# Optimization experiments

Measured on AMD Instinct MI355X. Metric: run time of the kernel, lower is better.

## Reference

```python
import jax, jax.numpy as jnp
import numpy as np

FREQUENCY_COUNT = 16

def setup_inputs() -> dict:
    key = jax.random.key(0)
    k1, k2 = jax.random.split(key)
    x = jax.random.normal(k1, (4096, 1024), dtype=jnp.float32)
    coef = jax.random.normal(k2, (1024, 1024, 2 * FREQUENCY_COUNT + 1), dtype=jnp.float32) * 0.1
    return {"x": x, "coef": coef}

def _fourier_features(x, K):
    ks = jnp.arange(1, K + 1, dtype=x.dtype)            # [K]
    ang = x[:, :, None] * ks[None, None, :]             # [B, I, K]
    ones = jnp.ones(x.shape + (1,), dtype=x.dtype)      # [B, I, 1]
    return jnp.concatenate([jnp.sin(ang), jnp.cos(ang), ones], axis=2)

def reference(x, coef):
    K = (coef.shape[-1] - 1) // 2
    values = _fourier_features(x, K)                     # [B, I, 2K+1]
    # sum over input dim i and frequency dim k, weighted per output j
    return jnp.einsum("oik,bik->bo", coef, values)      # [B, O]
```

## Files before the change

### kernel.cpp

```cpp
#include <hip/hip_runtime.h>


#define O_COLS 1024
#define I_DIM  1024
#define NFW    32
#define NF33   33
#define NIB    16
#define KPW    (NIB * NFW * 64)
#define CW_BYTES ((size_t)O_COLS * KPW * 2)

typedef _Float16 half8 __attribute__((ext_vector_type(8)));
typedef float float4v __attribute__((ext_vector_type(4)));
union H8 { half8 v; _Float16 h[8]; };

__device__ __forceinline__ void gload16(const void* g, void* l) {
  typedef const __attribute__((address_space(1))) unsigned int GU;
  typedef __attribute__((address_space(3))) unsigned int LU;
  __builtin_amdgcn_global_load_lds((GU*)g, (LU*)l, 16, 0, 0);
}

__device__ __forceinline__ int ksrc_of(int f) {
  return (f >= 32) ? 32 : ((f >> 1) + ((f & 1) ? 16 : 0));
}

__global__ __launch_bounds__(64)
void convert_coef(const float* __restrict__ coef, _Float16* __restrict__ Cw,
                  float* __restrict__ bias) {
  const int bid = blockIdx.x;
  const int o = bid >> 4;
  const int ib = bid & 15;
  const int j = threadIdx.x;
  const int i = ib * 64 + j;

  const float* src = coef + (size_t)o * (I_DIM * NF33) + (size_t)i * NF33;
  float r[NF33];
#pragma unroll
  for (int kk = 0; kk < NF33; ++kk) r[kk] = src[kk];

  const int c = j >> 3, e = j & 7;
  const int jswz = ((c ^ (o & 7)) << 3) + e;
  _Float16* dst = Cw + (size_t)o * KPW + (size_t)ib * (NFW * 64) + jswz;
#pragma unroll
  for (int f = 0; f < NFW; ++f) {
    dst[f * 64] = (_Float16)r[ksrc_of(f)];
  }

  float bsum = r[32];
#pragma unroll
  for (int off = 32; off > 0; off >>= 1) bsum += __shfl_down(bsum, off);
  if (j == 0) atomicAdd(&bias[o], bsum);
}

template <bool USE_WS>
__global__ __launch_bounds__(512, 4)
void fourier_gemm(const float* __restrict__ x, const float* __restrict__ coef,
                  const _Float16* __restrict__ Cw, const float* __restrict__ bias,
                  float* __restrict__ out) {
  __shared__ _Float16 As[128 * 64];
  __shared__ _Float16 Bs[128 * 64];

  const int tid = threadIdx.x;
  const int lane = tid & 63;
  const int wave = tid >> 6;
  const int wr = wave >> 1;
  const int wc = wave & 1;

  const int bid = blockIdx.x;
  const int o0 = (bid & 7) * 128;
  const int kb = (bid >> 3) & 1;
  const int m0 = (bid >> 4) * 128;

  const int rowA = tid >> 3;
  const int cch = tid & 7;
  const int cswz = cch ^ (rowA & 7);

  const int n1 = tid >> 3;
  const int c1q = tid & 7;

  const int r16 = lane & 15;
  const int kq = lane >> 4;

  const int NFG = USE_WS ? NFW : NF33;

  float4v acc[2][4];
#pragma unroll
  for (int fr = 0; fr < 2; ++fr)
#pragma unroll
    for (int fc = 0; fc < 4; ++fc)
      acc[fr][fc] = (float4v){0.f, 0.f, 0.f, 0.f};
  if (USE_WS && kb == 0) {
#pragma unroll
    for (int fc = 0; fc < 4; ++fc) {
      const float bv = bias[o0 + wc * 64 + fc * 16 + r16];
      acc[0][fc] = (float4v){bv, bv, bv, bv};
      acc[1][fc] = acc[0][fc];
    }
  }

  float s1a[8], c1a[8], sa[8], ca[8];
  float s1b[8], c1b[8], sb[8], cb[8];

  const float* xa_base = x + (size_t)(m0 + rowA) * I_DIM + (size_t)kb * 512 + cch * 8;
  const float* xb_base = xa_base + (size_t)64 * I_DIM;
  const _Float16* spB = Cw + (size_t)(o0 + n1) * KPW + (size_t)kb * 8 * (NFW * 64) + c1q * 8;

#pragma unroll 1
  for (int ib2 = 0; ib2 < 8; ++ib2) {
    {
      const float* xa = xa_base + ib2 * 64;
      const float* xb = xb_base + ib2 * 64;
      float xva[8], xvb[8];
      *(float4*)&xva[0] = *(const float4*)(xa);
      *(float4*)&xva[4] = *(const float4*)(xa + 4);
      *(float4*)&xvb[0] = *(const float4*)(xb);
      *(float4*)&xvb[4] = *(const float4*)(xb + 4);
#pragma unroll
      for (int e = 0; e < 8; ++e) {
        __sincosf(xva[e], &s1a[e], &c1a[e]);
        sa[e] = s1a[e]; ca[e] = c1a[e];
        __sincosf(xvb[e], &s1b[e], &c1b[e]);
        sb[e] = s1b[e]; cb[e] = c1b[e];
      }
    }

#pragma unroll 2
    for (int f = 0; f < NFG; ++f) {
      H8 ha, hb;
      if (!USE_WS && f == 32) {
#pragma unroll
        for (int e = 0; e < 8; ++e) { ha.h[e] = (_Float16)1.0f; hb.h[e] = (_Float16)1.0f; }
      } else if ((f & 1) == 0) {
#pragma unroll
        for (int e = 0; e < 8; ++e) { ha.h[e] = (_Float16)sa[e]; hb.h[e] = (_Float16)sb[e]; }
      } else {
#pragma unroll
        for (int e = 0; e < 8; ++e) { ha.h[e] = (_Float16)ca[e]; hb.h[e] = (_Float16)cb[e]; }
      }

      __syncthreads();

      if (USE_WS) {
        gload16(spB, (char*)Bs + wave * 1024);
        gload16(spB + (size_t)64 * KPW, (char*)Bs + 8192 + wave * 1024);
        spB += 64;
      } else {
        const int ks = ksrc_of(f);
        const int ibg = kb * 8 + ib2;
        H8 b1, b2;
#pragma unroll
        for (int e = 0; e < 8; ++e) {
          const size_t ii = (size_t)(ibg * 64 + c1q * 8 + e) * NF33 + ks;
          b1.h[e] = (_Float16)coef[(size_t)(o0 + n1) * (I_DIM * NF33) + ii];
          b2.h[e] = (_Float16)coef[(size_t)(o0 + n1 + 64) * (I_DIM * NF33) + ii];
        }
        const int cs = (c1q ^ (n1 & 7)) << 3;
        *(half8*)&Bs[n1 * 64 + cs] = b1.v;
        *(half8*)&Bs[(n1 + 64) * 64 + cs] = b2.v;
      }

      *(half8*)&As[rowA * 64 + cswz * 8] = ha.v;
      *(half8*)&As[(rowA + 64) * 64 + cswz * 8] = hb.v;

      if ((f & 1) && (f + 2 < NFG)) {
#pragma unroll
        for (int e = 0; e < 8; ++e) {
          float ns = sa[e] * c1a[e] + ca[e] * s1a[e];
          ca[e] = ca[e] * c1a[e] - sa[e] * s1a[e];
          sa[e] = ns;
          float nsb = sb[e] * c1b[e] + cb[e] * s1b[e];
          cb[e] = cb[e] * c1b[e] - sb[e] * s1b[e];
          sb[e] = nsb;
        }
      }

      __syncthreads();

#pragma unroll
      for (int ksu = 0; ksu < 2; ++ksu) {
        const int ch = ((ksu << 2) + kq) ^ (r16 & 7);
        half8 af[2], bf[4];
#pragma unroll
        for (int fr = 0; fr < 2; ++fr)
          af[fr] = *(const half8*)&As[(wr * 32 + fr * 16 + r16) * 64 + ch * 8];
#pragma unroll
        for (int fc = 0; fc < 4; ++fc)
          bf[fc] = *(const half8*)&Bs[(wc * 64 + fc * 16 + r16) * 64 + ch * 8];
#pragma unroll
        for (int fr = 0; fr < 2; ++fr)
#pragma unroll
          for (int fc = 0; fc < 4; ++fc)
            acc[fr][fc] = __builtin_amdgcn_mfma_f32_16x16x32_f16(
                af[fr], bf[fc], acc[fr][fc], 0, 0, 0);
      }
    }
  }

#pragma unroll
  for (int fr = 0; fr < 2; ++fr)
#pragma unroll
    for (int fc = 0; fc < 4; ++fc)
#pragma unroll
      for (int r = 0; r < 4; ++r) {
        const int row = m0 + wr * 32 + fr * 16 + kq * 4 + r;
        const int col = o0 + wc * 64 + fc * 16 + r16;
        atomicAdd(&out[(size_t)row * O_COLS + col], acc[fr][fc][r]);
      }
}

extern "C" void kernel_launch(void* const* d_in, const int* in_sizes, int n_in,
                              void* d_out, int out_size, void* d_ws, size_t ws_size,
                              hipStream_t stream) {
  const float* x = (const float*)d_in[0];
  const float* coef = (const float*)d_in[1];
  float* out = (float*)d_out;

  const bool use_ws = ws_size >= CW_BYTES + O_COLS * sizeof(float);

  hipMemsetAsync(d_out, 0, (size_t)4096 * O_COLS * sizeof(float), stream);

  if (use_ws) {
    _Float16* Cw = (_Float16*)d_ws;
    float* bias = (float*)((char*)d_ws + CW_BYTES);
    hipMemsetAsync(bias, 0, O_COLS * sizeof(float), stream);
    convert_coef<<<dim3(O_COLS * NIB), dim3(64), 0, stream>>>(coef, Cw, bias);
    fourier_gemm<true><<<dim3(512), dim3(512), 0, stream>>>(x, coef, Cw, bias, out);
  } else {
    fourier_gemm<false><<<dim3(512), dim3(512), 0, stream>>>(x, coef, nullptr, nullptr, out);
  }
}
```

Baseline: 409.5 us.

## Rewrite fourier GEMM with register-resident B fragments and 32x32 MFMA pipeline

Replaces the coefficient pre-pack with a new blob layout that lets each wave load its B fragments straight from global memory into registers, with no LDS staging. The main kernel now walks the input dimension one element at a time, builds the 16 harmonics per thread with sincos plus angle-addition recurrences, and double-buffers the A tile in LDS. It uses 32x32x16 MFMA with 256x128 tiles, a raw waitcnt barrier and setprio. The bias reduction moves to its own kernel without atomics. This trades a larger register footprint and lower occupancy (launch bound 2) for fewer LDS round trips and barriers.

```diff
diff --git a/kernel.cpp b/kernel.cpp
--- a/kernel.cpp
+++ b/kernel.cpp
@@ -3,61 +3,198 @@
 
 #define O_COLS 1024
 #define I_DIM  1024
-#define NFW    32
 #define NF33   33
-#define NIB    16
-#define KPW    (NIB * NFW * 64)
-#define CW_BYTES ((size_t)O_COLS * KPW * 2)
+#define NSTEP  512
+#define CW2_ELEMS ((size_t)32 * 2048 * 512)
+#define CW2_BYTES (CW2_ELEMS * 2)
 
 typedef _Float16 half8 __attribute__((ext_vector_type(8)));
-typedef float float4v __attribute__((ext_vector_type(4)));
+typedef float f32x16 __attribute__((ext_vector_type(16)));
 union H8 { half8 v; _Float16 h[8]; };
 
-__device__ __forceinline__ void gload16(const void* g, void* l) {
-  typedef const __attribute__((address_space(1))) unsigned int GU;
-  typedef __attribute__((address_space(3))) unsigned int LU;
-  __builtin_amdgcn_global_load_lds((GU*)g, (LU*)l, 16, 0, 0);
-}
+#define BAR() asm volatile("s_waitcnt lgkmcnt(0)\n\ts_barrier" ::: "memory")
 
 __device__ __forceinline__ int ksrc_of(int f) {
   return (f >= 32) ? 32 : ((f >> 1) + ((f & 1) ? 16 : 0));
 }
 
-__global__ __launch_bounds__(64)
-void convert_coef(const float* __restrict__ coef, _Float16* __restrict__ Cw,
-                  float* __restrict__ bias) {
-  const int bid = blockIdx.x;
-  const int o = bid >> 4;
-  const int ib = bid & 15;
-  const int j = threadIdx.x;
-  const int i = ib * 64 + j;
+__global__ __launch_bounds__(256)
+void convert_coef2(const float* __restrict__ coef, _Float16* __restrict__ Cw2) {
+  const int gtid = blockIdx.x * 256 + threadIdx.x;
+  const int o = gtid & 1023;
+  const int i = gtid >> 10;
 
   const float* src = coef + (size_t)o * (I_DIM * NF33) + (size_t)i * NF33;
   float r[NF33];
 #pragma unroll
-  for (int kk = 0; kk < NF33; ++kk) r[kk] = src[kk];
-
-  const int c = j >> 3, e = j & 7;
-  const int jswz = ((c ^ (o & 7)) << 3) + e;
-  _Float16* dst = Cw + (size_t)o * KPW + (size_t)ib * (NFW * 64) + jswz;
-#pragma unroll
-  for (int f = 0; f < NFW; ++f) {
-    dst[f * 64] = (_Float16)r[ksrc_of(f)];
-  }
-
-  float bsum = r[32];
-#pragma unroll
-  for (int off = 32; off > 0; off >>= 1) bsum += __shfl_down(bsum, off);
-  if (j == 0) atomicAdd(&bias[o], bsum);
-}
-
-template <bool USE_WS>
+  for (int k = 0; k < NF33; ++k) r[k] = src[k];
+
+  const int kb = i >> 9, il = i & 511;
+  const int ob32 = o >> 5;
+#pragma unroll
+  for (int fh = 0; fh < 2; ++fh) {
+#pragma unroll
+    for (int eh = 0; eh < 2; ++eh) {
+      H8 h;
+#pragma unroll
+      for (int e = 0; e < 8; ++e)
+        h.h[e] = (_Float16)r[ksrc_of(fh * 16 + eh * 8 + e)];
+      const size_t blob = (size_t)ob32 * 2048 + (size_t)kb * 1024 + il * 2 + fh;
+      *(half8*)(Cw2 + blob * 512 + (eh * 32 + (o & 31)) * 8) = h.v;
+    }
+  }
+}
+
+__global__ __launch_bounds__(256)
+void bias_kernel(const float* __restrict__ coef, float* __restrict__ bias) {
+  const int o = blockIdx.x, t = threadIdx.x;
+  float s = 0.f;
+#pragma unroll
+  for (int m = 0; m < 4; ++m)
+    s += coef[(size_t)o * (I_DIM * NF33) + (size_t)(t + 256 * m) * NF33 + 32];
+#pragma unroll
+  for (int off = 32; off > 0; off >>= 1) s += __shfl_down(s, off);
+  __shared__ float ps[4];
+  if ((t & 63) == 0) ps[t >> 6] = s;
+  __syncthreads();
+  if (t == 0) bias[o] = ps[0] + ps[1] + ps[2] + ps[3];
+}
+
+__global__ __launch_bounds__(512, 2)
+void fourier_gemm2(const float* __restrict__ x, const _Float16* __restrict__ Cw2,
+                   const float* __restrict__ bias, float* __restrict__ out) {
+  __shared__ _Float16 As[2][128 * 32];
+
+  const int tid = threadIdx.x;
+  const int lane = tid & 63;
+  const int wave = tid >> 6;
+  const int wr = wave & 1;
+  const int wc = wave >> 1;
+
+  const int bid = blockIdx.x;
+  const int g = bid & 7;
+  const int m0 = (bid >> 3) * 128;
+  const int o_t = g & 3;
+  const int kb = g >> 2;
+  const int o0 = o_t * 256;
+
+  const int rowW = tid >> 2;
+  const int jc = tid & 2 ? (tid & 3) : (tid & 3);
+  const int cw = (tid & 3) ^ (rowW & 3);
+  const float h1f = (float)(4 * (tid & 3) + 1);
+
+  const int r32 = lane & 31;
+  const int hf = lane >> 5;
+
+  const int ob32 = o_t * 8 + wc * 2;
+  const _Float16* pB0 = Cw2 + ((size_t)ob32 * 2048 + (size_t)kb * 1024) * 512 + lane * 8;
+  const _Float16* pB1 = pB0 + (size_t)2048 * 512;
+
+  const float* xrow = x + (size_t)(m0 + rowW) * I_DIM + kb * 512;
+
+  f32x16 acc[2][2];
+#pragma unroll
+  for (int fr = 0; fr < 2; ++fr)
+#pragma unroll
+    for (int fc = 0; fc < 2; ++fc)
+#pragma unroll
+      for (int q = 0; q < 16; ++q) acc[fr][fc][q] = 0.f;
+  if (kb == 0) {
+#pragma unroll
+    for (int fc = 0; fc < 2; ++fc) {
+      const float bv = bias[o0 + wc * 64 + fc * 32 + r32];
+#pragma unroll
+      for (int q = 0; q < 16; ++q) { acc[0][fc][q] = bv; acc[1][fc][q] = bv; }
+    }
+  }
+
+  half8 B0[4], B1[4];
+
+  auto loadB = [&](half8* Bt, int i) {
+    const size_t off = (size_t)i * 1024;
+#pragma unroll
+    for (int kcl = 0; kcl < 2; ++kcl) {
+      Bt[kcl]     = *(const half8*)(pB0 + off + kcl * 512);
+      Bt[2 + kcl] = *(const half8*)(pB1 + off + kcl * 512);
+    }
+  };
+
+  auto emitA = [&](int t, int pn) {
+    const float xc = xrow[t];
+    float s1, c1, sb, cb;
+    __sincosf(xc, &s1, &c1);
+    __sincosf(h1f * xc, &sb, &cb);
+    H8 h;
+    h.h[0] = (_Float16)sb; h.h[1] = (_Float16)cb;
+#pragma unroll
+    for (int q = 1; q < 4; ++q) {
+      const float ns = sb * c1 + cb * s1;
+      cb = cb * c1 - sb * s1;
+      sb = ns;
+      h.h[2 * q] = (_Float16)sb; h.h[2 * q + 1] = (_Float16)cb;
+    }
+    *(half8*)&As[pn][rowW * 32 + cw * 8] = h.v;
+  };
+
+  auto compute = [&](int pn, const half8* Bt) {
+    half8 af[2][2];
+#pragma unroll
+    for (int kcl = 0; kcl < 2; ++kcl)
+#pragma unroll
+      for (int fr = 0; fr < 2; ++fr) {
+        const int row = wr * 64 + fr * 32 + r32;
+        const int c = (kcl * 2 + hf) ^ (r32 & 3);
+        af[fr][kcl] = *(const half8*)&As[pn][row * 32 + c * 8];
+      }
+    __builtin_amdgcn_s_setprio(1);
+#pragma unroll
+    for (int kcl = 0; kcl < 2; ++kcl)
+#pragma unroll
+      for (int fr = 0; fr < 2; ++fr)
+#pragma unroll
+        for (int fc = 0; fc < 2; ++fc)
+          acc[fr][fc] = __builtin_amdgcn_mfma_f32_32x32x16_f16(
+              af[fr][kcl], Bt[fc * 2 + kcl], acc[fr][fc], 0, 0, 0);
+    __builtin_amdgcn_s_setprio(0);
+  };
+
+  emitA(0, 0);
+  loadB(B0, 0);
+  BAR();
+
+#pragma unroll 1
+  for (int s = 0; s < NSTEP; s += 2) {
+    loadB(B1, s + 1);
+    emitA(s + 1, 1);
+    compute(0, B0);
+    BAR();
+    if (s + 2 < NSTEP) {
+      loadB(B0, s + 2);
+      emitA(s + 2, 0);
+    }
+    compute(1, B1);
+    BAR();
+  }
+
+#pragma unroll
+  for (int fr = 0; fr < 2; ++fr)
+#pragma unroll
+    for (int fc = 0; fc < 2; ++fc)
+#pragma unroll
+      for (int q = 0; q < 16; ++q) {
+        const int row = m0 + wr * 64 + fr * 32 + (q & 3) + 8 * (q >> 2) + 4 * hf;
+        const int col = o0 + wc * 64 + fc * 32 + r32;
+        atomicAdd(&out[(size_t)row * O_COLS + col], acc[fr][fc][q]);
+      }
+}
+
+typedef float float4v __attribute__((ext_vector_type(4)));
+
 __global__ __launch_bounds__(512, 4)
-void fourier_gemm(const float* __restrict__ x, const float* __restrict__ coef,
-                  const _Float16* __restrict__ Cw, const float* __restrict__ bias,
-                  float* __restrict__ out) {
-  __shared__ _Float16 As[128 * 64];
-  __shared__ _Float16 Bs[128 * 64];
+void fourier_gemm_direct(const float* __restrict__ x, const float* __restrict__ coef,
+                         float* __restrict__ out) {
+  __shared__ _Float16 Asd[128 * 64];
+  __shared__ _Float16 Bsd[128 * 64];
 
   const int tid = threadIdx.x;
   const int lane = tid & 63;
@@ -73,36 +210,22 @@
   const int rowA = tid >> 3;
   const int cch = tid & 7;
   const int cswz = cch ^ (rowA & 7);
-
   const int n1 = tid >> 3;
   const int c1q = tid & 7;
-
   const int r16 = lane & 15;
   const int kq = lane >> 4;
 
-  const int NFG = USE_WS ? NFW : NF33;
-
   float4v acc[2][4];
 #pragma unroll
   for (int fr = 0; fr < 2; ++fr)
 #pragma unroll
-    for (int fc = 0; fc < 4; ++fc)
-      acc[fr][fc] = (float4v){0.f, 0.f, 0.f, 0.f};
-  if (USE_WS && kb == 0) {
-#pragma unroll
-    for (int fc = 0; fc < 4; ++fc) {
-      const float bv = bias[o0 + wc * 64 + fc * 16 + r16];
-      acc[0][fc] = (float4v){bv, bv, bv, bv};
-      acc[1][fc] = acc[0][fc];
-    }
-  }
+    for (int fc = 0; fc < 4; ++fc) acc[fr][fc] = (float4v){0.f, 0.f, 0.f, 0.f};
 
   float s1a[8], c1a[8], sa[8], ca[8];
   float s1b[8], c1b[8], sb[8], cb[8];
 
   const float* xa_base = x + (size_t)(m0 + rowA) * I_DIM + (size_t)kb * 512 + cch * 8;
   const float* xb_base = xa_base + (size_t)64 * I_DIM;
-  const _Float16* spB = Cw + (size_t)(o0 + n1) * KPW + (size_t)kb * 8 * (NFW * 64) + c1q * 8;
 
 #pragma unroll 1
   for (int ib2 = 0; ib2 < 8; ++ib2) {
@@ -116,17 +239,14 @@
       *(float4*)&xvb[4] = *(const float4*)(xb + 4);
 #pragma unroll
       for (int e = 0; e < 8; ++e) {
-        __sincosf(xva[e], &s1a[e], &c1a[e]);
-        sa[e] = s1a[e]; ca[e] = c1a[e];
-        __sincosf(xvb[e], &s1b[e], &c1b[e]);
-        sb[e] = s1b[e]; cb[e] = c1b[e];
-      }
-    }
-
-#pragma unroll 2
-    for (int f = 0; f < NFG; ++f) {
+        __sincosf(xva[e], &s1a[e], &c1a[e]); sa[e] = s1a[e]; ca[e] = c1a[e];
+        __sincosf(xvb[e], &s1b[e], &c1b[e]); sb[e] = s1b[e]; cb[e] = c1b[e];
+      }
+    }
+#pragma unroll 1
+    for (int f = 0; f < NF33; ++f) {
       H8 ha, hb;
-      if (!USE_WS && f == 32) {
+      if (f == 32) {
 #pragma unroll
         for (int e = 0; e < 8; ++e) { ha.h[e] = (_Float16)1.0f; hb.h[e] = (_Float16)1.0f; }
       } else if ((f & 1) == 0) {
@@ -136,14 +256,8 @@
 #pragma unroll
         for (int e = 0; e < 8; ++e) { ha.h[e] = (_Float16)ca[e]; hb.h[e] = (_Float16)cb[e]; }
       }
-
       __syncthreads();
-
-      if (USE_WS) {
-        gload16(spB, (char*)Bs + wave * 1024);
-        gload16(spB + (size_t)64 * KPW, (char*)Bs + 8192 + wave * 1024);
-        spB += 64;
-      } else {
+      {
         const int ks = ksrc_of(f);
         const int ibg = kb * 8 + ib2;
         H8 b1, b2;
@@ -154,37 +268,31 @@
           b2.h[e] = (_Float16)coef[(size_t)(o0 + n1 + 64) * (I_DIM * NF33) + ii];
         }
         const int cs = (c1q ^ (n1 & 7)) << 3;
-        *(half8*)&Bs[n1 * 64 + cs] = b1.v;
-        *(half8*)&Bs[(n1 + 64) * 64 + cs] = b2.v;
-      }
-
-      *(half8*)&As[rowA * 64 + cswz * 8] = ha.v;
-      *(half8*)&As[(rowA + 64) * 64 + cswz * 8] = hb.v;
-
-      if ((f & 1) && (f + 2 < NFG)) {
+        *(half8*)&Bsd[n1 * 64 + cs] = b1.v;
+        *(half8*)&Bsd[(n1 + 64) * 64 + cs] = b2.v;
+      }
+      *(half8*)&Asd[rowA * 64 + cswz * 8] = ha.v;
+      *(half8*)&Asd[(rowA + 64) * 64 + cswz * 8] = hb.v;
+      if ((f & 1) && (f + 2 < NF33)) {
 #pragma unroll
         for (int e = 0; e < 8; ++e) {
           float ns = sa[e] * c1a[e] + ca[e] * s1a[e];
-          ca[e] = ca[e] * c1a[e] - sa[e] * s1a[e];
-          sa[e] = ns;
+          ca[e] = ca[e] * c1a[e] - sa[e] * s1a[e]; sa[e] = ns;
           float nsb = sb[e] * c1b[e] + cb[e] * s1b[e];
-          cb[e] = cb[e] * c1b[e] - sb[e] * s1b[e];
-          sb[e] = nsb;
+          cb[e] = cb[e] * c1b[e] - sb[e] * s1b[e]; sb[e] = nsb;
         }
       }
-
       __syncthreads();
-
 #pragma unroll
       for (int ksu = 0; ksu < 2; ++ksu) {
         const int ch = ((ksu << 2) + kq) ^ (r16 & 7);
         half8 af[2], bf[4];
 #pragma unroll
         for (int fr = 0; fr < 2; ++fr)
-          af[fr] = *(const half8*)&As[(wr * 32 + fr * 16 + r16) * 64 + ch * 8];
+          af[fr] = *(const half8*)&Asd[(wr * 32 + fr * 16 + r16) * 64 + ch * 8];
 #pragma unroll
         for (int fc = 0; fc < 4; ++fc)
-          bf[fc] = *(const half8*)&Bs[(wc * 64 + fc * 16 + r16) * 64 + ch * 8];
+          bf[fc] = *(const half8*)&Bsd[(wc * 64 + fc * 16 + r16) * 64 + ch * 8];
 #pragma unroll
         for (int fr = 0; fr < 2; ++fr)
 #pragma unroll
@@ -194,7 +302,6 @@
       }
     }
   }
-
 #pragma unroll
   for (int fr = 0; fr < 2; ++fr)
 #pragma unroll
@@ -214,17 +321,15 @@
   const float* coef = (const float*)d_in[1];
   float* out = (float*)d_out;
 
-  const bool use_ws = ws_size >= CW_BYTES + O_COLS * sizeof(float);
-
   hipMemsetAsync(d_out, 0, (size_t)4096 * O_COLS * sizeof(float), stream);
 
-  if (use_ws) {
-    _Float16* Cw = (_Float16*)d_ws;
-    float* bias = (float*)((char*)d_ws + CW_BYTES);
-    hipMemsetAsync(bias, 0, O_COLS * sizeof(float), stream);
-    convert_coef<<<dim3(O_COLS * NIB), dim3(64), 0, stream>>>(coef, Cw, bias);
-    fourier_gemm<true><<<dim3(512), dim3(512), 0, stream>>>(x, coef, Cw, bias, out);
+  if (ws_size >= CW2_BYTES + O_COLS * sizeof(float)) {
+    _Float16* Cw2 = (_Float16*)d_ws;
+    float* bias = (float*)((char*)d_ws + CW2_BYTES);
+    convert_coef2<<<dim3(4096), dim3(256), 0, stream>>>(coef, Cw2);
+    bias_kernel<<<dim3(O_COLS), dim3(256), 0, stream>>>(coef, bias);
+    fourier_gemm2<<<dim3(256), dim3(512), 0, stream>>>(x, Cw2, bias, out);
   } else {
-    fourier_gemm<false><<<dim3(512), dim3(512), 0, stream>>>(x, coef, nullptr, nullptr, out);
-  }
-}
+    fourier_gemm_direct<<<dim3(512), dim3(512), 0, stream>>>(x, coef, out);
+  }
+}
```

Result: slower. 513.4 us (+25.4%).
